# Optimization experiments

Measured on AMD Instinct MI355X. Metric: run time of the kernel, lower is better.

The kernel has to match this reference:

```python
import jax, jax.numpy as jnp
import numpy as np

N, C, H, W = 512, 2048, 16, 8
NUM_CLASSES = 751
ALPHA = 1.2      # margin
LAMB = 0.5       # self.l
SIGMA = 0.8      # osm_sigma
BN_EPS = 1e-5


def setup_inputs() -> dict:
    key = jax.random.key(0)
    k1, k2, k3 = jax.random.split(key, 3)
    features = jax.random.normal(k1, (N, C, H, W), dtype=jnp.float32)
    targets = jax.random.randint(k2, (N,), 0, NUM_CLASSES)
    gamma = jnp.ones((C,), dtype=jnp.float32)  # BN weight, init 1 (weights_init_kaiming)
    # kaiming_uniform_(a=sqrt(5)) on [NUM_CLASSES, C]: bound = 1/sqrt(C)
    bound = 1.0 / np.sqrt(C)
    weight = jax.random.uniform(k3, (NUM_CLASSES, C), jnp.float32, -bound, bound)
    return {"features": features, "targets": targets, "gamma": gamma, "weight": weight}


def _l2norm(x, axis=-1):
    return x / jnp.maximum(jnp.linalg.norm(x, axis=axis, keepdims=True), 1e-12)


def reference(features, targets, gamma, weight):
    n = features.shape[0]
    # AdaptiveAvgPool2d(1) + Flatten
    global_feat = jnp.mean(features, axis=(2, 3))  # [n, C]
    # NoBiasBatchNorm1d (training mode: batch stats, biased var, no bias)
    mu = jnp.mean(global_feat, axis=0)
    var = jnp.var(global_feat, axis=0)
    bn_feat = (global_feat - mu) / jnp.sqrt(var + BN_EPS) * gamma
    bn_feat = _l2norm(bn_feat, axis=1)  # F.normalize

    # pairwise euclidean distance
    sq = jnp.sum(bn_feat * bn_feat, axis=1)                       # [n]
    dist2 = sq[:, None] + sq[None, :] - 2.0 * (bn_feat @ bn_feat.T)
    dist = jnp.sqrt(jnp.clip(dist2, 1e-12, None))                 # [n, n]

    S_pos = jnp.exp(-(dist * dist) / (SIGMA * SIGMA))
    S_neg = jnp.clip(ALPHA - dist, 1e-12, None)
    p_mask = targets[:, None] == targets[None, :]                 # [n, n] bool
    S = jnp.where(p_mask, S_pos, S_neg)

    # per-sample attention: exp(logits)[i, t_i] / sum_j exp(logits)[i, j] == softmax
    logits = bn_feat @ _l2norm(weight, axis=1).T                  # [n, num_classes]
    probs = jax.nn.softmax(logits, axis=1)
    atten = probs[jnp.arange(n), targets]                         # [n]
    A = jnp.minimum(atten[None, :], atten[:, None])               # [n, n]

    Wmat = S * A
    off_diag = 1.0 - jnp.eye(n, dtype=Wmat.dtype)
    W_P = Wmat * p_mask.astype(Wmat.dtype) * off_diag
    W_N = Wmat * (~p_mask).astype(Wmat.dtype) * off_diag

    L_P = 0.5 * jnp.sum(W_P * dist * dist) / jnp.sum(W_P)
    L_N = 0.5 * jnp.sum(W_N * S_neg * S_neg) / jnp.sum(W_N)
    L = (1.0 - LAMB) * L_P + LAMB * L_N
    return (L, global_feat)
```

## Files before the change

kernel.cpp:

```cpp
#include <hip/hip_runtime.h>
#include <hip/hip_bf16.h>
#include <math.h>

#define N_S   512
#define C_S   2048
#define HW_S  128
#define NCLS  751
#define NCLSP 768
#define ALPHA 1.2f
#define LAMB  0.5f
#define SIGMA 0.8f
#define BN_EPS 1e-5f
#define KSPLIT 4
#define KSEG  (C_S / KSPLIT)

typedef __attribute__((ext_vector_type(8))) short short8;
typedef __attribute__((ext_vector_type(4))) float f32x4;

__device__ __forceinline__ unsigned short f2bf(float x) {
    __hip_bfloat16 h = __float2bfloat16(x);
    return *reinterpret_cast<unsigned short*>(&h);
}

__global__ __launch_bounds__(256) void pool_kernel(const float* __restrict__ feat,
                                                   float* __restrict__ out_gf,
                                                   float* __restrict__ ctrl) {
    if (blockIdx.x == 0 && threadIdx.x < 8) ctrl[threadIdx.x] = 0.0f;
    int pair = blockIdx.x * 32 + (threadIdx.x >> 3);
    int sub  = threadIdx.x & 7;
    const f32x4* p = reinterpret_cast<const f32x4*>(feat + (size_t)pair * HW_S);
    f32x4 v0 = __builtin_nontemporal_load(p + sub);
    f32x4 v1 = __builtin_nontemporal_load(p + sub + 8);
    f32x4 v2 = __builtin_nontemporal_load(p + sub + 16);
    f32x4 v3 = __builtin_nontemporal_load(p + sub + 24);
    float s = (v0[0] + v0[1] + v0[2] + v0[3]) + (v1[0] + v1[1] + v1[2] + v1[3])
            + (v2[0] + v2[1] + v2[2] + v2[3]) + (v3[0] + v3[1] + v3[2] + v3[3]);
    #pragma unroll
    for (int off = 4; off > 0; off >>= 1) s += __shfl_down(s, off, 8);
    if (sub == 0) out_gf[pair] = s * (1.0f / HW_S);
}

__global__ __launch_bounds__(256) void meanvar_kernel(const float* __restrict__ gf,
                                                      const float* __restrict__ gamma,
                                                      float* __restrict__ mu_out,
                                                      float* __restrict__ scale_out) {
    int tc = threadIdx.x & 31;
    int tr = threadIdx.x >> 5;
    int c  = blockIdx.x * 32 + tc;
    const float* col = gf + c;
    float sum = 0.f, sumsq = 0.f;
    #pragma unroll 4
    for (int n = tr * 64; n < tr * 64 + 64; ++n) {
        float x = col[(size_t)n * C_S];
        sum += x; sumsq += x * x;
    }
    __shared__ float s1[8][32], s2[8][32];
    s1[tr][tc] = sum; s2[tr][tc] = sumsq;
    __syncthreads();
    if (threadIdx.x < 32) {
        int cc = blockIdx.x * 32 + threadIdx.x;
        float a = 0.f, b = 0.f;
        #pragma unroll
        for (int r = 0; r < 8; ++r) { a += s1[r][threadIdx.x]; b += s2[r][threadIdx.x]; }
        float mu  = a * (1.0f / N_S);
        float var = b * (1.0f / N_S) - mu * mu;
        mu_out[cc]    = mu;
        scale_out[cc] = gamma[cc] / sqrtf(var + BN_EPS);
    }
}

__global__ __launch_bounds__(256) void norm_kernel(const float* __restrict__ gf,
                                                   const float* __restrict__ mu,
                                                   const float* __restrict__ scale,
                                                   const float* __restrict__ w,
                                                   unsigned short* __restrict__ bnnh,
                                                   unsigned short* __restrict__ wnh,
                                                   float* __restrict__ sq) {
    int b = blockIdx.x, t = threadIdx.x;
    __shared__ float red[4];
    __shared__ float sinv;
    if (b < N_S) {
        int n = b;
        const float* row = gf + (size_t)n * C_S;
        float v[8]; float ss = 0.f;
        #pragma unroll
        for (int k = 0; k < 8; ++k) {
            int c = t + k * 256;
            float x = (row[c] - mu[c]) * scale[c];
            v[k] = x; ss += x * x;
        }
        #pragma unroll
        for (int off = 32; off > 0; off >>= 1) ss += __shfl_down(ss, off, 64);
        if ((t & 63) == 0) red[t >> 6] = ss;
        __syncthreads();
        if (t == 0) {
            float tot = red[0] + red[1] + red[2] + red[3];
            float inv = 1.0f / fmaxf(sqrtf(tot), 1e-12f);
            sinv = inv;
            sq[n] = tot * inv * inv;
        }
        __syncthreads();
        float inv = sinv;
        unsigned short* orow = bnnh + (size_t)n * C_S;
        #pragma unroll
        for (int k = 0; k < 8; ++k) orow[t + k * 256] = f2bf(v[k] * inv);
    } else {
        int r = b - N_S;
        unsigned short* orow = wnh + (size_t)r * C_S;
        if (r >= NCLS) {
            #pragma unroll
            for (int k = 0; k < 8; ++k) orow[t + k * 256] = 0;
            return;
        }
        const float* row = w + (size_t)r * C_S;
        float v[8]; float ss = 0.f;
        #pragma unroll
        for (int k = 0; k < 8; ++k) {
            float x = row[t + k * 256];
            v[k] = x; ss += x * x;
        }
        #pragma unroll
        for (int off = 32; off > 0; off >>= 1) ss += __shfl_down(ss, off, 64);
        if ((t & 63) == 0) red[t >> 6] = ss;
        __syncthreads();
        if (t == 0) sinv = 1.0f / fmaxf(sqrtf(red[0]+red[1]+red[2]+red[3]), 1e-12f);
        __syncthreads();
        float inv = sinv;
        #pragma unroll
        for (int k = 0; k < 8; ++k) orow[t + k * 256] = f2bf(v[k] * inv);
    }
}

__global__ __launch_bounds__(256) void gemm_kernel(const unsigned short* __restrict__ bnnh,
                                                   const unsigned short* __restrict__ wnh,
                                                   float* __restrict__ logits_p,
                                                   float* __restrict__ G_p) {
    int wave = threadIdx.x >> 6, lane = threadIdx.x & 63;
    int gid = blockIdx.x * 4 + wave;
    const unsigned short* Bh; float* Cm; int m0, n0, ldc, ks;
    if (gid < 1536) {
        int tile = gid >> 2; ks = gid & 3;
        Bh = wnh; m0 = (tile & 31) * 16; n0 = (tile >> 5) * 64; ldc = NCLSP;
        Cm = logits_p + (size_t)ks * (N_S * NCLSP);
    } else {
        int g2 = gid - 1536;
        int tile = g2 >> 2; ks = g2 & 3;
        Bh = bnnh; m0 = (tile & 31) * 16; n0 = (tile >> 5) * 64; ldc = N_S;
        Cm = G_p + (size_t)ks * (N_S * N_S);
    }
    int kbase = ks * KSEG;
    int mrow = m0 + (lane & 15);
    int kq   = (lane >> 4) * 8;
    f32x4 acc0 = {0,0,0,0}, acc1 = {0,0,0,0}, acc2 = {0,0,0,0}, acc3 = {0,0,0,0};
    const unsigned short* arow = bnnh + (size_t)mrow * C_S + kbase + kq;
    const unsigned short* brow = Bh + (size_t)(n0 + (lane & 15)) * C_S + kbase + kq;
    #pragma unroll 4
    for (int k = 0; k < KSEG; k += 32) {
        short8 a  = *reinterpret_cast<const short8*>(arow + k);
        short8 b0 = *reinterpret_cast<const short8*>(brow + k);
        short8 b1 = *reinterpret_cast<const short8*>(brow + 16 * C_S + k);
        short8 b2 = *reinterpret_cast<const short8*>(brow + 32 * C_S + k);
        short8 b3 = *reinterpret_cast<const short8*>(brow + 48 * C_S + k);
        acc0 = __builtin_amdgcn_mfma_f32_16x16x32_bf16(a, b0, acc0, 0, 0, 0);
        acc1 = __builtin_amdgcn_mfma_f32_16x16x32_bf16(a, b1, acc1, 0, 0, 0);
        acc2 = __builtin_amdgcn_mfma_f32_16x16x32_bf16(a, b2, acc2, 0, 0, 0);
        acc3 = __builtin_amdgcn_mfma_f32_16x16x32_bf16(a, b3, acc3, 0, 0, 0);
    }
    int ccol  = lane & 15;
    int crow0 = m0 + (lane >> 4) * 4;
    #pragma unroll
    for (int r = 0; r < 4; ++r) {
        float* orow = Cm + (size_t)(crow0 + r) * ldc + n0 + ccol;
        orow[0]  = acc0[r];
        orow[16] = acc1[r];
        orow[32] = acc2[r];
        orow[48] = acc3[r];
    }
}

__global__ __launch_bounds__(256) void softmax_atten_kernel(const float* __restrict__ logits_p,
                                                            const int* __restrict__ targets,
                                                            float* __restrict__ atten) {
    int n = blockIdx.x, t = threadIdx.x;
    const f32x4* r0 = reinterpret_cast<const f32x4*>(logits_p + (size_t)n * NCLSP);
    const f32x4* r1 = r0 + (size_t)(N_S * NCLSP) / 4;
    const f32x4* r2 = r1 + (size_t)(N_S * NCLSP) / 4;
    const f32x4* r3 = r2 + (size_t)(N_S * NCLSP) / 4;
    __shared__ float red[4];
    __shared__ float srmax, srsum, stgt;
    const bool has = (t < NCLSP / 4);
    f32x4 v = {-1e30f, -1e30f, -1e30f, -1e30f};
    float m = -1e30f;
    if (has) {
        f32x4 a = r0[t], b = r1[t], c = r2[t], d = r3[t];
        v = a + b + c + d;
        int base = t * 4;
        if (base + 0 >= NCLS) v[0] = -1e30f;
        if (base + 1 >= NCLS) v[1] = -1e30f;
        if (base + 2 >= NCLS) v[2] = -1e30f;
        if (base + 3 >= NCLS) v[3] = -1e30f;
        m = fmaxf(fmaxf(v[0], v[1]), fmaxf(v[2], v[3]));
    }
    #pragma unroll
    for (int off = 32; off > 0; off >>= 1) m = fmaxf(m, __shfl_down(m, off, 64));
    if ((t & 63) == 0) red[t >> 6] = m;
    __syncthreads();
    if (t == 0) srmax = fmaxf(fmaxf(red[0], red[1]), fmaxf(red[2], red[3]));
    __syncthreads();
    float rm = srmax;
    int tg = targets[n];
    float s = 0.f;
    if (has) {
        float ex = expf(v[0] - rm);
        float ey = expf(v[1] - rm);
        float ez = expf(v[2] - rm);
        float ew = expf(v[3] - rm);
        s = ex + ey + ez + ew;
        if (t == (tg >> 2)) {
            int e = tg & 3;
            stgt = (e == 0) ? ex : (e == 1) ? ey : (e == 2) ? ez : ew;
        }
    }
    #pragma unroll
    for (int off = 32; off > 0; off >>= 1) s += __shfl_down(s, off, 64);
    if ((t & 63) == 0) red[t >> 6] = s;
    __syncthreads();
    if (t == 0) {
        srsum = red[0] + red[1] + red[2] + red[3];
        atten[n] = stgt / srsum;
    }
}

__global__ __launch_bounds__(256) void pair_reduce_kernel(const float* __restrict__ G_p,
                                                          const float* __restrict__ sq,
                                                          const float* __restrict__ atten,
                                                          const int* __restrict__ targets,
                                                          float* __restrict__ ctrl,
                                                          float* __restrict__ out) {
    float numP = 0.f, denP = 0.f, numN = 0.f, denN = 0.f;
    const float inv_sig2 = 1.0f / (SIGMA * SIGMA);
    int g  = blockIdx.x * 256 + threadIdx.x;
    int i  = g >> 7;
    int j0 = (g & 127) * 4;
    size_t p = (size_t)i * N_S + j0;
    const f32x4* G0 = reinterpret_cast<const f32x4*>(G_p + p);
    const f32x4* G1 = reinterpret_cast<const f32x4*>(G_p + N_S * N_S + p);
    const f32x4* G2 = reinterpret_cast<const f32x4*>(G_p + 2 * N_S * N_S + p);
    const f32x4* G3 = reinterpret_cast<const f32x4*>(G_p + 3 * N_S * N_S + p);
    f32x4 gsumv = *G0 + *G1 + *G2 + *G3;
    float gsum[4] = { gsumv[0], gsumv[1], gsumv[2], gsumv[3] };
    f32x4 sqjv = *reinterpret_cast<const f32x4*>(sq + j0);
    float sqj[4] = { sqjv[0], sqjv[1], sqjv[2], sqjv[3] };
    f32x4 ajv = *reinterpret_cast<const f32x4*>(atten + j0);
    float aj[4] = { ajv[0], ajv[1], ajv[2], ajv[3] };
    int4 tjv = *reinterpret_cast<const int4*>(targets + j0);
    int tj[4] = { tjv.x, tjv.y, tjv.z, tjv.w };
    float sqi = sq[i];
    float ai  = atten[i];
    int   ti  = targets[i];
    #pragma unroll
    for (int e = 0; e < 4; ++e) {
        if (i == j0 + e) continue;
        float d2   = fmaxf(sqi + sqj[e] - 2.0f * gsum[e], 1e-12f);
        float dist = sqrtf(d2);
        float sneg = fmaxf(ALPHA - dist, 1e-12f);
        float Aij  = fminf(ai, aj[e]);
        if (ti == tj[e]) {
            float Wm = expf(-d2 * inv_sig2) * Aij;
            numP += Wm * d2; denP += Wm;
        } else {
            float Wm = sneg * Aij;
            numN += Wm * sneg * sneg; denN += Wm;
        }
    }
    #pragma unroll
    for (int off = 32; off > 0; off >>= 1) {
        numP += __shfl_down(numP, off, 64);
        denP += __shfl_down(denP, off, 64);
        numN += __shfl_down(numN, off, 64);
        denN += __shfl_down(denN, off, 64);
    }
    __shared__ float red[4][4];
    int t = threadIdx.x;
    if ((t & 63) == 0) {
        int w = t >> 6;
        red[w][0] = numP; red[w][1] = denP; red[w][2] = numN; red[w][3] = denN;
    }
    __syncthreads();
    if (t < 4) {
        float s = red[0][t] + red[1][t] + red[2][t] + red[3][t];
        atomicAdd(&ctrl[t], s);
    }
    __syncthreads();
    if (t == 0) {
        __threadfence();
        unsigned prev = atomicAdd(reinterpret_cast<unsigned*>(ctrl + 4), 1u);
        if (prev == gridDim.x - 1) {
            float a0 = atomicAdd(&ctrl[0], 0.0f);
            float a1 = atomicAdd(&ctrl[1], 0.0f);
            float a2 = atomicAdd(&ctrl[2], 0.0f);
            float a3 = atomicAdd(&ctrl[3], 0.0f);
            float L_P = 0.5f * a0 / a1;
            float L_N = 0.5f * a2 / a3;
            out[0] = (1.0f - LAMB) * L_P + LAMB * L_N;
        }
    }
}

extern "C" void kernel_launch(void* const* d_in, const int* in_sizes, int n_in,
                              void* d_out, int out_size, void* d_ws, size_t ws_size,
                              hipStream_t stream) {
    const float* features = (const float*)d_in[0];
    const int*   targets  = (const int*)d_in[1];
    const float* gamma    = (const float*)d_in[2];
    const float* weight   = (const float*)d_in[3];
    float* out = (float*)d_out;
    float* gf  = out + 1;

    float* ws       = (float*)d_ws;
    float* mu       = ws;
    float* scale    = mu + 2048;
    float* sq       = scale + 2048;
    float* atten    = sq + 512;
    float* ctrl     = atten + 512;
    float* logits_p = ctrl + 16;
    float* G_p      = logits_p + 4 * (N_S * NCLSP);
    unsigned short* bnnh = (unsigned short*)(G_p + 4 * (N_S * N_S));
    unsigned short* wnh  = bnnh + (size_t)N_S * C_S;

    hipLaunchKernelGGL(pool_kernel, dim3((N_S * C_S) / 32), dim3(256), 0, stream,
                       features, gf, ctrl);
    hipLaunchKernelGGL(meanvar_kernel, dim3(C_S / 32), dim3(256), 0, stream,
                       gf, gamma, mu, scale);
    hipLaunchKernelGGL(norm_kernel, dim3(N_S + NCLSP), dim3(256), 0, stream,
                       gf, mu, scale, weight, bnnh, wnh, sq);
    hipLaunchKernelGGL(gemm_kernel, dim3(640), dim3(256), 0, stream,
                       bnnh, wnh, logits_p, G_p);
    hipLaunchKernelGGL(softmax_atten_kernel, dim3(N_S), dim3(256), 0, stream,
                       logits_p, targets, atten);
    hipLaunchKernelGGL(pair_reduce_kernel, dim3(256), dim3(256), 0, stream,
                       G_p, sq, atten, targets, ctrl, out);
}
```

Measured before the change: 708.1 us.

## Reduce GEMM split-K partials in LDS and vectorize norm kernel loads/stores

The four split-K waves of each GEMM block now cover one output tile together. They sum their partials through shared memory and write a single vectorized result, where before each wave wrote a separate partial buffer that the softmax and pair kernels had to re-read and add. This removes the 4x partial global writes and reads for logits and the Gram matrix. The norm kernel also switches to 128-bit vector loads and short8 stores. The cost is extra LDS use and a block-level barrier in the GEMM epilogue.

```diff
diff --git a/kernel.cpp b/kernel.cpp
--- a/kernel.cpp
+++ b/kernel.cpp
@@ -81,14 +81,13 @@
     __shared__ float sinv;
     if (b < N_S) {
         int n = b;
-        const float* row = gf + (size_t)n * C_S;
-        float v[8]; float ss = 0.f;
-        #pragma unroll
-        for (int k = 0; k < 8; ++k) {
-            int c = t + k * 256;
-            float x = (row[c] - mu[c]) * scale[c];
-            v[k] = x; ss += x * x;
-        }
+        const f32x4* rowv = reinterpret_cast<const f32x4*>(gf + (size_t)n * C_S + t * 8);
+        const f32x4* muv  = reinterpret_cast<const f32x4*>(mu + t * 8);
+        const f32x4* scv  = reinterpret_cast<const f32x4*>(scale + t * 8);
+        f32x4 v0 = (rowv[0] - muv[0]) * scv[0];
+        f32x4 v1 = (rowv[1] - muv[1]) * scv[1];
+        float ss = v0[0]*v0[0] + v0[1]*v0[1] + v0[2]*v0[2] + v0[3]*v0[3]
+                 + v1[0]*v1[0] + v1[1]*v1[1] + v1[2]*v1[2] + v1[3]*v1[3];
         #pragma unroll
         for (int off = 32; off > 0; off >>= 1) ss += __shfl_down(ss, off, 64);
         if ((t & 63) == 0) red[t >> 6] = ss;
@@ -101,24 +100,23 @@
         }
         __syncthreads();
         float inv = sinv;
-        unsigned short* orow = bnnh + (size_t)n * C_S;
-        #pragma unroll
-        for (int k = 0; k < 8; ++k) orow[t + k * 256] = f2bf(v[k] * inv);
+        short8 o;
+        #pragma unroll
+        for (int k = 0; k < 4; ++k) o[k]     = (short)f2bf(v0[k] * inv);
+        #pragma unroll
+        for (int k = 0; k < 4; ++k) o[4 + k] = (short)f2bf(v1[k] * inv);
+        *reinterpret_cast<short8*>(bnnh + (size_t)n * C_S + t * 8) = o;
     } else {
         int r = b - N_S;
-        unsigned short* orow = wnh + (size_t)r * C_S;
         if (r >= NCLS) {
-            #pragma unroll
-            for (int k = 0; k < 8; ++k) orow[t + k * 256] = 0;
+            short8 z = {0,0,0,0,0,0,0,0};
+            *reinterpret_cast<short8*>(wnh + (size_t)r * C_S + t * 8) = z;
             return;
         }
-        const float* row = w + (size_t)r * C_S;
-        float v[8]; float ss = 0.f;
-        #pragma unroll
-        for (int k = 0; k < 8; ++k) {
-            float x = row[t + k * 256];
-            v[k] = x; ss += x * x;
-        }
+        const f32x4* rowv = reinterpret_cast<const f32x4*>(w + (size_t)r * C_S + t * 8);
+        f32x4 v0 = rowv[0], v1 = rowv[1];
+        float ss = v0[0]*v0[0] + v0[1]*v0[1] + v0[2]*v0[2] + v0[3]*v0[3]
+                 + v1[0]*v1[0] + v1[1]*v1[1] + v1[2]*v1[2] + v1[3]*v1[3];
         #pragma unroll
         for (int off = 32; off > 0; off >>= 1) ss += __shfl_down(ss, off, 64);
         if ((t & 63) == 0) red[t >> 6] = ss;
@@ -126,29 +124,31 @@
         if (t == 0) sinv = 1.0f / fmaxf(sqrtf(red[0]+red[1]+red[2]+red[3]), 1e-12f);
         __syncthreads();
         float inv = sinv;
-        #pragma unroll
-        for (int k = 0; k < 8; ++k) orow[t + k * 256] = f2bf(v[k] * inv);
+        short8 o;
+        #pragma unroll
+        for (int k = 0; k < 4; ++k) o[k]     = (short)f2bf(v0[k] * inv);
+        #pragma unroll
+        for (int k = 0; k < 4; ++k) o[4 + k] = (short)f2bf(v1[k] * inv);
+        *reinterpret_cast<short8*>(wnh + (size_t)r * C_S + t * 8) = o;
     }
 }
 
 __global__ __launch_bounds__(256) void gemm_kernel(const unsigned short* __restrict__ bnnh,
                                                    const unsigned short* __restrict__ wnh,
-                                                   float* __restrict__ logits_p,
-                                                   float* __restrict__ G_p) {
+                                                   float* __restrict__ logits,
+                                                   float* __restrict__ G) {
     int wave = threadIdx.x >> 6, lane = threadIdx.x & 63;
-    int gid = blockIdx.x * 4 + wave;
-    const unsigned short* Bh; float* Cm; int m0, n0, ldc, ks;
-    if (gid < 1536) {
-        int tile = gid >> 2; ks = gid & 3;
-        Bh = wnh; m0 = (tile & 31) * 16; n0 = (tile >> 5) * 64; ldc = NCLSP;
-        Cm = logits_p + (size_t)ks * (N_S * NCLSP);
+    int gid = blockIdx.x;
+    const unsigned short* Bh; float* Cm; int m0, n0, ldc;
+    if (gid < 384) {
+        Bh = wnh; m0 = (gid & 31) * 16; n0 = (gid >> 5) * 64; ldc = NCLSP;
+        Cm = logits;
     } else {
-        int g2 = gid - 1536;
-        int tile = g2 >> 2; ks = g2 & 3;
-        Bh = bnnh; m0 = (tile & 31) * 16; n0 = (tile >> 5) * 64; ldc = N_S;
-        Cm = G_p + (size_t)ks * (N_S * N_S);
-    }
-    int kbase = ks * KSEG;
+        int g2 = gid - 384;
+        Bh = bnnh; m0 = (g2 & 31) * 16; n0 = (g2 >> 5) * 64; ldc = N_S;
+        Cm = G;
+    }
+    int kbase = wave * KSEG;
     int mrow = m0 + (lane & 15);
     int kq   = (lane >> 4) * 8;
     f32x4 acc0 = {0,0,0,0}, acc1 = {0,0,0,0}, acc2 = {0,0,0,0}, acc3 = {0,0,0,0};
@@ -166,34 +166,41 @@
         acc2 = __builtin_amdgcn_mfma_f32_16x16x32_bf16(a, b2, acc2, 0, 0, 0);
         acc3 = __builtin_amdgcn_mfma_f32_16x16x32_bf16(a, b3, acc3, 0, 0, 0);
     }
-    int ccol  = lane & 15;
-    int crow0 = m0 + (lane >> 4) * 4;
+    __shared__ float lds[4][16 * 68];
+    int lrow = (lane >> 4) * 4;
+    int lcol = lane & 15;
     #pragma unroll
     for (int r = 0; r < 4; ++r) {
-        float* orow = Cm + (size_t)(crow0 + r) * ldc + n0 + ccol;
-        orow[0]  = acc0[r];
-        orow[16] = acc1[r];
-        orow[32] = acc2[r];
-        orow[48] = acc3[r];
-    }
-}
-
-__global__ __launch_bounds__(256) void softmax_atten_kernel(const float* __restrict__ logits_p,
+        float* dst = &lds[wave][(lrow + r) * 68 + lcol];
+        dst[0]  = acc0[r];
+        dst[16] = acc1[r];
+        dst[32] = acc2[r];
+        dst[48] = acc3[r];
+    }
+    __syncthreads();
+    int t   = threadIdx.x;
+    int row = t >> 4;
+    int col = (t & 15) * 4;
+    const f32x4* p0 = reinterpret_cast<const f32x4*>(&lds[0][row * 68 + col]);
+    const f32x4* p1 = reinterpret_cast<const f32x4*>(&lds[1][row * 68 + col]);
+    const f32x4* p2 = reinterpret_cast<const f32x4*>(&lds[2][row * 68 + col]);
+    const f32x4* p3 = reinterpret_cast<const f32x4*>(&lds[3][row * 68 + col]);
+    f32x4 s = *p0 + *p1 + *p2 + *p3;
+    *reinterpret_cast<f32x4*>(Cm + (size_t)(m0 + row) * ldc + n0 + col) = s;
+}
+
+__global__ __launch_bounds__(256) void softmax_atten_kernel(const float* __restrict__ logits,
                                                             const int* __restrict__ targets,
                                                             float* __restrict__ atten) {
     int n = blockIdx.x, t = threadIdx.x;
-    const f32x4* r0 = reinterpret_cast<const f32x4*>(logits_p + (size_t)n * NCLSP);
-    const f32x4* r1 = r0 + (size_t)(N_S * NCLSP) / 4;
-    const f32x4* r2 = r1 + (size_t)(N_S * NCLSP) / 4;
-    const f32x4* r3 = r2 + (size_t)(N_S * NCLSP) / 4;
+    const f32x4* r0 = reinterpret_cast<const f32x4*>(logits + (size_t)n * NCLSP);
     __shared__ float red[4];
     __shared__ float srmax, srsum, stgt;
     const bool has = (t < NCLSP / 4);
     f32x4 v = {-1e30f, -1e30f, -1e30f, -1e30f};
     float m = -1e30f;
     if (has) {
-        f32x4 a = r0[t], b = r1[t], c = r2[t], d = r3[t];
-        v = a + b + c + d;
+        v = r0[t];
         int base = t * 4;
         if (base + 0 >= NCLS) v[0] = -1e30f;
         if (base + 1 >= NCLS) v[1] = -1e30f;
@@ -231,7 +238,7 @@
     }
 }
 
-__global__ __launch_bounds__(256) void pair_reduce_kernel(const float* __restrict__ G_p,
+__global__ __launch_bounds__(256) void pair_reduce_kernel(const float* __restrict__ G,
                                                           const float* __restrict__ sq,
                                                           const float* __restrict__ atten,
                                                           const int* __restrict__ targets,
@@ -243,11 +250,7 @@
     int i  = g >> 7;
     int j0 = (g & 127) * 4;
     size_t p = (size_t)i * N_S + j0;
-    const f32x4* G0 = reinterpret_cast<const f32x4*>(G_p + p);
-    const f32x4* G1 = reinterpret_cast<const f32x4*>(G_p + N_S * N_S + p);
-    const f32x4* G2 = reinterpret_cast<const f32x4*>(G_p + 2 * N_S * N_S + p);
-    const f32x4* G3 = reinterpret_cast<const f32x4*>(G_p + 3 * N_S * N_S + p);
-    f32x4 gsumv = *G0 + *G1 + *G2 + *G3;
+    f32x4 gsumv = *reinterpret_cast<const f32x4*>(G + p);
     float gsum[4] = { gsumv[0], gsumv[1], gsumv[2], gsumv[3] };
     f32x4 sqjv = *reinterpret_cast<const f32x4*>(sq + j0);
     float sqj[4] = { sqjv[0], sqjv[1], sqjv[2], sqjv[3] };
@@ -317,15 +320,15 @@
     float* out = (float*)d_out;
     float* gf  = out + 1;
 
-    float* ws       = (float*)d_ws;
-    float* mu       = ws;
-    float* scale    = mu + 2048;
-    float* sq       = scale + 2048;
-    float* atten    = sq + 512;
-    float* ctrl     = atten + 512;
-    float* logits_p = ctrl + 16;
-    float* G_p      = logits_p + 4 * (N_S * NCLSP);
-    unsigned short* bnnh = (unsigned short*)(G_p + 4 * (N_S * N_S));
+    float* ws     = (float*)d_ws;
+    float* mu     = ws;
+    float* scale  = mu + 2048;
+    float* sq     = scale + 2048;
+    float* atten  = sq + 512;
+    float* ctrl   = atten + 512;
+    float* logits = ctrl + 16;
+    float* G      = logits + (size_t)N_S * NCLSP;
+    unsigned short* bnnh = (unsigned short*)(G + (size_t)N_S * N_S);
     unsigned short* wnh  = bnnh + (size_t)N_S * C_S;
 
     hipLaunchKernelGGL(pool_kernel, dim3((N_S * C_S) / 32), dim3(256), 0, stream,
@@ -335,9 +338,9 @@
     hipLaunchKernelGGL(norm_kernel, dim3(N_S + NCLSP), dim3(256), 0, stream,
                        gf, mu, scale, weight, bnnh, wnh, sq);
     hipLaunchKernelGGL(gemm_kernel, dim3(640), dim3(256), 0, stream,
-                       bnnh, wnh, logits_p, G_p);
+                       bnnh, wnh, logits, G);
     hipLaunchKernelGGL(softmax_atten_kernel, dim3(N_S), dim3(256), 0, stream,
-                       logits_p, targets, atten);
+                       logits, targets, atten);
     hipLaunchKernelGGL(pair_reduce_kernel, dim3(256), dim3(256), 0, stream,
-                       G_p, sq, atten, targets, ctrl, out);
-}
+                       G, sq, atten, targets, ctrl, out);
+}
```

Result: no change. 706.6 us (-0.2%).
